# Optimization experiments

Hardware: AMD Instinct MI355X
Metric: run time of the kernel (lower is better)

## Reference

```python
import jax, jax.numpy as jnp
import numpy as np

EPS = 1e-7
K_IN, K_HID, K_OUT = 1.0, 1.1, 1.2
N_NODES, N_EDGES, IN_DIM, HID = 50000, 400000, 1024, 1024


def _expmap0(u, k):
    # u: tangent at origin with time component 0; u[:, 1:] are spatial coords
    sqrtK = jnp.sqrt(k)
    us = u[:, 1:]
    un = jnp.maximum(jnp.linalg.norm(us, axis=1, keepdims=True), EPS)
    t = un / sqrtK
    return jnp.concatenate([sqrtK * jnp.cosh(t), sqrtK * jnp.sinh(t) * us / un], axis=1)


def _logmap0(x, k):
    sqrtK = jnp.sqrt(k)
    x0, xs = x[:, 0:1], x[:, 1:]
    xn = jnp.maximum(jnp.linalg.norm(xs, axis=1, keepdims=True), EPS)
    theta = jnp.maximum(x0 / sqrtK, 1.0 + EPS)
    d = sqrtK * jnp.arccosh(theta)
    return jnp.concatenate([jnp.zeros_like(x0), d * xs / xn], axis=1)


def _proj(x, k):
    # re-fix the time component so <x,x>_L = -k
    xs = x[:, 1:]
    x0 = jnp.sqrt(k + jnp.sum(xs * xs, axis=1, keepdims=True))
    return jnp.concatenate([x0, xs], axis=1)


def _centroid(m, k):
    # Lorentzian centroid normalization: sqrt(k) * m / sqrt(|<m,m>_L|)
    l_inner = jnp.sum(m[:, 1:] ** 2, axis=1, keepdims=True) - m[:, 0:1] ** 2
    denom = jnp.sqrt(jnp.maximum(jnp.abs(l_inner), EPS))
    return jnp.sqrt(k) * m / denom


def _lgcn_conv(x, W, b, edge_src, edge_dst, edge_w, k_in, k_out):
    n = x.shape[0]
    # Lorentzian linear: logmap0 -> spatial matmul + bias -> expmap0
    u = _logmap0(x, k_in)[:, 1:]                      # [N, in_f]
    mx = u @ W.T + b                                  # [N, out_f-1]
    h = _expmap0(jnp.concatenate([jnp.zeros_like(mx[:, :1]), mx], axis=1), k_in)
    # sparse neighborhood aggregation + Lorentzian centroid
    msgs = edge_w[:, None] * h[edge_src]              # [E, out_f]
    m = jax.ops.segment_sum(msgs, edge_dst, num_segments=n)
    h = _centroid(m, k_in)
    # Lorentzian activation: relu in tangent space, re-exp on output manifold
    t = jax.nn.relu(_logmap0(h, k_in))                # time comp stays 0
    return _proj(_expmap0(t, k_out), k_out)


def setup_inputs() -> dict:
    key = jax.random.key(0)
    ks = jax.random.split(key, 8)
    x = jax.random.normal(ks[0], (N_NODES, IN_DIM), jnp.float32) * 0.01
    edge_src = jax.random.randint(ks[1], (N_EDGES,), 0, N_NODES, jnp.int32)
    edge_dst = jax.random.randint(ks[2], (N_EDGES,), 0, N_NODES, jnp.int32)
    edge_w = jax.random.uniform(ks[3], (N_EDGES,), jnp.float32)
    W1 = jax.random.normal(ks[4], (HID - 1, IN_DIM), jnp.float32) * 0.02
    b1 = jax.random.normal(ks[5], (HID - 1,), jnp.float32) * 0.01
    W2 = jax.random.normal(ks[6], (HID - 1, HID - 1), jnp.float32) * 0.02
    b2 = jax.random.normal(ks[7], (HID - 1,), jnp.float32) * 0.01
    return {"x": x, "edge_src": edge_src, "edge_dst": edge_dst, "edge_w": edge_w,
            "W1": W1, "b1": b1, "W2": W2, "b2": b2}


def reference(x, edge_src, edge_dst, edge_w, W1, b1, W2, b2):
    # encode(): prepend zero time coord, proj_tan0 (already 0), expmap0, proj
    x = jnp.concatenate([jnp.zeros_like(x[:, :1]), x], axis=1)  # [N, IN_DIM+1]
    xh = _proj(_expmap0(x, K_IN), K_IN)
    x1 = _lgcn_conv(xh, W1, b1, edge_src, edge_dst, edge_w, K_IN, K_HID)
    y = _lgcn_conv(x1, W2, b2, edge_src, edge_dst, edge_w, K_HID, K_OUT)
    return y
```

## Files before the change

kernel.cpp:

```cpp
#include <hip/hip_runtime.h>
#include <math.h>

#define EPSF 1e-7f
#define KPAD 1024
#define M_PAD 50176
#define NWG2 784

typedef __attribute__((ext_vector_type(8))) short bf16x8;
typedef __attribute__((ext_vector_type(4))) float f32x4;
typedef __attribute__((ext_vector_type(4))) unsigned short us4;
typedef __attribute__((ext_vector_type(8))) unsigned short us8;

__device__ inline unsigned short f2bf(float f) {
  unsigned u = __float_as_uint(f);
  return (unsigned short)((u + 0x7FFFu + ((u >> 16) & 1u)) >> 16);
}
__device__ inline float bf2f(unsigned short s) {
  return __uint_as_float(((unsigned)s) << 16);
}

__device__ inline void gload_lds16(const void* g, void* l) {
  __builtin_amdgcn_global_load_lds((const __attribute__((address_space(1))) void*)g,
                                   (__attribute__((address_space(3))) void*)l, 16, 0, 0);
}

__global__ __launch_bounds__(256) void cvt_rows_bf16(const float* __restrict__ x,
                                                     unsigned short* __restrict__ o) {
  int i = blockIdx.x, t = threadIdx.x;
  float4 v = *(const float4*)(x + (size_t)i * 1024 + 4 * t);
  us4 u = {f2bf(v.x), f2bf(v.y), f2bf(v.z), f2bf(v.w)};
  *(us4*)(o + (size_t)i * 1024 + 4 * t) = u;
}

__global__ __launch_bounds__(256) void cvt_w_bf16(const float* __restrict__ W,
                                                  unsigned short* __restrict__ o,
                                                  int rows, int cols) {
  int r = blockIdx.x, t = threadIdx.x;
  int c0 = 4 * t;
  us4 u;
#pragma unroll
  for (int j = 0; j < 4; ++j) {
    int c = c0 + j;
    float v = (r < rows && c < cols) ? W[(size_t)r * cols + c] : 0.0f;
    u[j] = f2bf(v);
  }
  *(us4*)(o + (size_t)r * 1024 + c0) = u;
}

__global__ __launch_bounds__(512, 2) void gemm_bt256(const unsigned short* __restrict__ A,
                                                     const unsigned short* __restrict__ B,
                                                     const float* __restrict__ bias,
                                                     unsigned short* __restrict__ C,
                                                     float* __restrict__ rowss) {
  __shared__ unsigned short lA[2 * 2 * 8192];
  __shared__ unsigned short lB[2 * 2 * 8192];
  const int wg = blockIdx.x;
  const int swz = (wg & 7) * 98 + (wg >> 3);
  const int bm = swz >> 2, bn = swz & 3;
  const int tid = threadIdx.x;
  const int wave = tid >> 6, lane = tid & 63;
  const int wr = wave >> 2, wc = wave & 3;
  const int fr = lane & 15, fg = lane >> 4;

  const unsigned short* Abase = A + (size_t)bm * 256 * KPAD;
  const unsigned short* Bbase = B + (size_t)bn * 256 * KPAD;

  const int aHalf = wr * 8192;
  const int bHalf = (wc >> 1) * 8192;
  const int lrB0 = (wc & 1) * 64;
  int ps[2];
#pragma unroll
  for (int s = 0; s < 2; ++s) ps[s] = (((s << 2) + fg) ^ (fr & 7)) << 3;

  const int sRow8 = lane >> 3;
  const int sDst = wave * 512 + lane * 8;
  const int sGran = ((lane & 7) ^ sRow8) << 3;

  f32x4 acc[8][4];
#pragma unroll
  for (int m = 0; m < 8; ++m)
#pragma unroll
    for (int n2 = 0; n2 < 4; ++n2) acc[m][n2] = (f32x4)0.0f;

  bf16x8 af[4][2], bf[4][2];

  auto STAGE_A = [&](int t, int h) {
    const int p = t & 1;
#pragma unroll
    for (int q = 0; q < 2; ++q) {
      int row = h * 128 + q * 64 + wave * 8 + sRow8;
      gload_lds16(Abase + (size_t)row * KPAD + t * 64 + sGran,
                  &lA[p * 16384 + h * 8192 + q * 4096 + sDst]);
    }
  };
  auto STAGE_B = [&](int t, int h) {
    const int p = t & 1;
#pragma unroll
    for (int q = 0; q < 2; ++q) {
      int row = h * 128 + q * 64 + wave * 8 + sRow8;
      gload_lds16(Bbase + (size_t)row * KPAD + t * 64 + sGran,
                  &lB[p * 16384 + h * 8192 + q * 4096 + sDst]);
    }
  };
  auto LDA4 = [&](int p, int mg) {
#pragma unroll
    for (int mi = 0; mi < 4; ++mi) {
      int ro = p * 16384 + aHalf + ((mg * 4 + mi) * 16 + fr) * 64;
#pragma unroll
      for (int s = 0; s < 2; ++s) af[mi][s] = *(const bf16x8*)&lA[ro + ps[s]];
    }
  };
  auto LDB2 = [&](int p, int ng) {
#pragma unroll
    for (int ni = 0; ni < 2; ++ni) {
      int ro = p * 16384 + bHalf + (lrB0 + (ng * 2 + ni) * 16 + fr) * 64;
#pragma unroll
      for (int s = 0; s < 2; ++s) bf[ng * 2 + ni][s] = *(const bf16x8*)&lB[ro + ps[s]];
    }
  };
  auto MM = [&](int mq, int nq) {
    __builtin_amdgcn_s_setprio(1);
#pragma unroll
    for (int mi = 0; mi < 4; ++mi)
#pragma unroll
      for (int ni = 0; ni < 2; ++ni)
#pragma unroll
        for (int s = 0; s < 2; ++s)
          acc[mq * 4 + mi][nq * 2 + ni] = __builtin_amdgcn_mfma_f32_16x16x32_bf16(
              af[mi][s], bf[nq * 2 + ni][s], acc[mq * 4 + mi][nq * 2 + ni], 0, 0, 0);
    __builtin_amdgcn_s_setprio(0);
  };
#define BAR() __builtin_amdgcn_s_barrier()

  STAGE_B(0, 0); STAGE_B(0, 1); STAGE_A(0, 0); STAGE_A(0, 1);
  STAGE_B(1, 0); STAGE_B(1, 1); STAGE_A(1, 0);
  asm volatile("s_waitcnt vmcnt(6)" ::: "memory");
  BAR();

#pragma unroll 1
  for (int it = 0; it < 7; ++it) {
    const int t0 = 2 * it, t1 = t0 + 1;
    LDA4(0, 0); LDB2(0, 0);
    STAGE_A(t1, 1);
    BAR(); MM(0, 0); BAR();
    LDB2(0, 1);
    BAR(); MM(0, 1); BAR();
    LDA4(0, 1);
    STAGE_B(t0 + 2, 0);
    BAR(); MM(1, 0); BAR();
    STAGE_B(t0 + 2, 1); STAGE_A(t0 + 2, 0);
    asm volatile("s_waitcnt vmcnt(6)" ::: "memory");
    BAR(); MM(1, 1); BAR();
    LDA4(1, 0); LDB2(1, 0);
    STAGE_A(t0 + 2, 1);
    BAR(); MM(0, 0); BAR();
    LDB2(1, 1);
    BAR(); MM(0, 1); BAR();
    LDA4(1, 1);
    STAGE_B(t1 + 2, 0);
    BAR(); MM(1, 0); BAR();
    STAGE_B(t1 + 2, 1); STAGE_A(t1 + 2, 0);
    asm volatile("s_waitcnt vmcnt(6)" ::: "memory");
    BAR(); MM(1, 1); BAR();
  }

  asm volatile("s_waitcnt vmcnt(0)" ::: "memory");
  BAR();
#pragma unroll
  for (int p = 0; p < 2; ++p) {
    LDA4(p, 0); LDB2(p, 0); MM(0, 0);
    LDB2(p, 1); MM(0, 1);
    LDA4(p, 1); MM(1, 0); MM(1, 1);
  }
#undef BAR

  const int crow0 = bm * 256 + wr * 128;
  const int ccol0 = bn * 256 + wc * 64;
  float rs[8][4];
#pragma unroll
  for (int m = 0; m < 8; ++m)
#pragma unroll
    for (int j = 0; j < 4; ++j) rs[m][j] = 0.0f;
#pragma unroll
  for (int m = 0; m < 8; ++m) {
#pragma unroll
    for (int n2 = 0; n2 < 4; ++n2) {
      int col = ccol0 + n2 * 16 + fr;
      float bv = (col < 1023) ? bias[col] : 0.0f;
      int row0 = crow0 + m * 16 + fg * 4;
      unsigned short* cp = C + (size_t)row0 * 1024 + col;
#pragma unroll
      for (int j = 0; j < 4; ++j) {
        float v = acc[m][n2][j] + bv;
        cp[(size_t)j * 1024] = f2bf(v);
        rs[m][j] += v * v;
      }
    }
  }
#pragma unroll
  for (int m = 0; m < 8; ++m)
#pragma unroll
    for (int j = 0; j < 4; ++j) {
      float v = rs[m][j];
      v += __shfl_xor(v, 1);
      v += __shfl_xor(v, 2);
      v += __shfl_xor(v, 4);
      v += __shfl_xor(v, 8);
      rs[m][j] = v;
    }
  __syncthreads();
  float* red = (float*)lA;
  if (fr == 0) {
#pragma unroll
    for (int m = 0; m < 8; ++m)
#pragma unroll
      for (int j = 0; j < 4; ++j)
        red[(wr * 128 + m * 16 + fg * 4 + j) * 4 + wc] = rs[m][j];
  }
  __syncthreads();
  if (tid < 256) {
    float s = red[tid * 4] + red[tid * 4 + 1] + red[tid * 4 + 2] + red[tid * 4 + 3];
    rowss[(size_t)(bm * 256 + tid) * 4 + bn] = s;
  }
}

__global__ __launch_bounds__(256) void row_finalize(const float* __restrict__ rowss,
                                                    unsigned short* __restrict__ raw,
                                                    float* __restrict__ sc_tab, float sqrtK,
                                                    int n) {
  int i = blockIdx.x * 256 + threadIdx.x;
  if (i >= n) return;
  float ss = rowss[4 * i] + rowss[4 * i + 1] + rowss[4 * i + 2] + rowss[4 * i + 3];
  float un = fmaxf(sqrtf(ss), EPSF);
  float tt = un / sqrtK;
  float e = expf(tt);
  float ch = 0.5f * (e + 1.0f / e), sh = 0.5f * (e - 1.0f / e);
  float h0 = sqrtK * ch, sc = sqrtK * sh / un;
  sc_tab[i] = sc;
  raw[(size_t)i * 1024 + 1023] = f2bf(h0 / sc);
}

__global__ __launch_bounds__(256) void deg_count(const int* __restrict__ ed, int* __restrict__ cnt,
                                                 int nE) {
  int i = blockIdx.x * 256 + threadIdx.x;
  if (i < nE) atomicAdd(&cnt[ed[i]], 1);
}

__global__ __launch_bounds__(256) void scan1(const int* __restrict__ cnt, int* __restrict__ excl,
                                             int* __restrict__ bsum, int n) {
  __shared__ int s[256];
  int t = threadIdx.x;
  int i = blockIdx.x * 256 + t;
  int v = (i < n) ? cnt[i] : 0;
  s[t] = v;
  __syncthreads();
#pragma unroll
  for (int o = 1; o < 256; o <<= 1) {
    int add = (t >= o) ? s[t - o] : 0;
    __syncthreads();
    s[t] += add;
    __syncthreads();
  }
  if (i < n) excl[i] = s[t] - v;
  if (t == 255) bsum[blockIdx.x] = s[t];
}

__global__ __launch_bounds__(256) void scan2(int* __restrict__ bsum, int* __restrict__ boff,
                                             int nb) {
  __shared__ int s[256];
  int t = threadIdx.x;
  int v = (t < nb) ? bsum[t] : 0;
  s[t] = v;
  __syncthreads();
#pragma unroll
  for (int o = 1; o < 256; o <<= 1) {
    int add = (t >= o) ? s[t - o] : 0;
    __syncthreads();
    s[t] += add;
    __syncthreads();
  }
  if (t < nb) boff[t] = s[t] - v;
}

__global__ __launch_bounds__(256) void scan3(int* __restrict__ excl, const int* __restrict__ boff,
                                             int* __restrict__ rowstart, int* __restrict__ fill,
                                             int n, int nE) {
  int i = blockIdx.x * 256 + threadIdx.x;
  if (i < n) {
    int v = excl[i] + boff[blockIdx.x];
    rowstart[i] = v;
    fill[i] = v;
  }
  if (i == 0) rowstart[n] = nE;
}

__global__ __launch_bounds__(256) void bucket_fill(const int* __restrict__ es,
                                                   const int* __restrict__ ed,
                                                   const float* __restrict__ ew,
                                                   int* __restrict__ fill,
                                                   int2* __restrict__ sedge, int nE) {
  int i = blockIdx.x * 256 + threadIdx.x;
  if (i < nE) {
    int d = ed[i];
    int pos = atomicAdd(&fill[d], 1);
    sedge[pos] = make_int2(es[i], __float_as_int(ew[i]));
  }
}

__device__ inline void gather_row_wave(const unsigned short* __restrict__ h,
                                       const float* __restrict__ sc,
                                       const int2* __restrict__ sedge, int j0, int j1,
                                       int lane, float* fa, float* fb) {
  const char* hb = (const char*)h;
  int j = j0;
  for (; j + 2 <= j1; j += 2) {
    int2 e0 = sedge[j], e1 = sedge[j + 1];
    float w0 = __int_as_float(e0.y) * sc[e0.x];
    float w1 = __int_as_float(e1.y) * sc[e1.x];
    const us8* p0 = (const us8*)(hb + (((unsigned)e0.x) << 11)) + lane;
    const us8* p1 = (const us8*)(hb + (((unsigned)e1.x) << 11)) + lane;
    us8 a0 = p0[0], b0 = p0[64];
    us8 a1 = p1[0], b1 = p1[64];
#pragma unroll
    for (int q = 0; q < 8; ++q) {
      fa[q] += w0 * bf2f(a0[q]) + w1 * bf2f(a1[q]);
      fb[q] += w0 * bf2f(b0[q]) + w1 * bf2f(b1[q]);
    }
  }
  if (j < j1) {
    int2 e = sedge[j];
    float w = __int_as_float(e.y) * sc[e.x];
    const us8* p = (const us8*)(hb + (((unsigned)e.x) << 11)) + lane;
    us8 a = p[0], b = p[64];
#pragma unroll
    for (int q = 0; q < 8; ++q) {
      fa[q] += w * bf2f(a[q]);
      fb[q] += w * bf2f(b[q]);
    }
  }
}

__device__ inline float wave_sum(float v) {
#pragma unroll
  for (int m = 1; m <= 32; m <<= 1) v += __shfl_xor(v, m);
  return v;
}

__global__ __launch_bounds__(256) void gather_centroid_tangent(
    const unsigned short* __restrict__ h, const float* __restrict__ sc,
    const int* __restrict__ rs, const int2* __restrict__ sedge,
    unsigned short* __restrict__ u16, float sqrtK, int n) {
  int wv = threadIdx.x >> 6, lane = threadIdx.x & 63;
  int i = blockIdx.x * 4 + wv;
  if (i >= n) return;
  int j0 = rs[i], j1 = rs[i + 1];
  float fa[8] = {0.f, 0.f, 0.f, 0.f, 0.f, 0.f, 0.f, 0.f};
  float fb[8] = {0.f, 0.f, 0.f, 0.f, 0.f, 0.f, 0.f, 0.f};
  gather_row_wave(h, sc, sedge, j0, j1, lane, fa, fb);
  float m0 = __shfl(fb[7], 63);
  if (lane == 63) fb[7] = 0.0f;
  float ssl = 0.f;
#pragma unroll
  for (int q = 0; q < 8; ++q) ssl += fa[q] * fa[q] + fb[q] * fb[q];
  float ss = wave_sum(ssl);

  float l = ss - m0 * m0;
  float denom = sqrtf(fmaxf(fabsf(l), EPSF));
  float c = sqrtK / denom;
  float xn = fmaxf(c * sqrtf(ss), EPSF);
  float theta = fmaxf(m0 / denom, 1.0f + EPSF);
  float d = sqrtK * acoshf(theta);
  float f = c * (d / xn);
  us8 ua, ub;
#pragma unroll
  for (int q = 0; q < 8; ++q) {
    ua[q] = f2bf(fmaxf(fa[q], 0.0f) * f);
    ub[q] = f2bf(fmaxf(fb[q], 0.0f) * f);
  }
  if (lane == 63) ub[7] = 0;
  unsigned short* o = u16 + (size_t)i * 1024 + lane * 8;
  *(us8*)o = ua;
  *(us8*)(o + 512) = ub;
}

__global__ __launch_bounds__(256) void gather_centroid_final(
    const unsigned short* __restrict__ h, const float* __restrict__ sc,
    const int* __restrict__ rs, const int2* __restrict__ sedge, float* __restrict__ y,
    float sqrtKin, float sqrtKout, int n) {
  int wv = threadIdx.x >> 6, lane = threadIdx.x & 63;
  int i = blockIdx.x * 4 + wv;
  if (i >= n) return;
  int j0 = rs[i], j1 = rs[i + 1];
  float fa[8] = {0.f, 0.f, 0.f, 0.f, 0.f, 0.f, 0.f, 0.f};
  float fb[8] = {0.f, 0.f, 0.f, 0.f, 0.f, 0.f, 0.f, 0.f};
  gather_row_wave(h, sc, sedge, j0, j1, lane, fa, fb);
  float m0 = __shfl(fb[7], 63);
  if (lane == 63) fb[7] = 0.0f;
  float ssl = 0.f;
#pragma unroll
  for (int q = 0; q < 8; ++q) ssl += fa[q] * fa[q] + fb[q] * fb[q];
  float ss = wave_sum(ssl);

  float l = ss - m0 * m0;
  float denom = sqrtf(fmaxf(fabsf(l), EPSF));
  float c = sqrtKin / denom;
  float xn = fmaxf(c * sqrtf(ss), EPSF);
  float theta = fmaxf(m0 / denom, 1.0f + EPSF);
  float d = sqrtKin * acoshf(theta);
  float f = c * (d / xn);
  float oa[8], ob[8];
  float ss2l = 0.f;
#pragma unroll
  for (int q = 0; q < 8; ++q) {
    oa[q] = fmaxf(fa[q], 0.0f) * f;
    ob[q] = fmaxf(fb[q], 0.0f) * f;
  }
  if (lane == 63) ob[7] = 0.0f;
#pragma unroll
  for (int q = 0; q < 8; ++q) ss2l += oa[q] * oa[q] + ob[q] * ob[q];
  float ss2 = wave_sum(ss2l);

  float un = fmaxf(sqrtf(ss2), EPSF);
  float tt = un / sqrtKout;
  float e = expf(tt);
  float ch = 0.5f * (e + 1.0f / e), sh = 0.5f * (e - 1.0f / e);
  float y0 = sqrtKout * ch, scale = sqrtKout * sh / un;
  float* yr = y + (size_t)i * 1024;
  int c0 = lane * 8;
#pragma unroll
  for (int q = 0; q < 8; ++q) {
    yr[1 + c0 + q] = scale * oa[q];
    int colb = 512 + c0 + q;
    if (colb < 1023) yr[1 + colb] = scale * ob[q];
  }
  if (lane == 0) yr[0] = y0;
}

extern "C" void kernel_launch(void* const* d_in, const int* in_sizes, int n_in,
                              void* d_out, int out_size, void* d_ws, size_t ws_size,
                              hipStream_t stream) {
  const float* x = (const float*)d_in[0];
  const int* es = (const int*)d_in[1];
  const int* ed = (const int*)d_in[2];
  const float* ew = (const float*)d_in[3];
  const float* W1 = (const float*)d_in[4];
  const float* b1 = (const float*)d_in[5];
  const float* W2 = (const float*)d_in[6];
  const float* b2 = (const float*)d_in[7];
  float* y = (float*)d_out;

  const int n = in_sizes[0] / 1024;
  const int nE = in_sizes[1];
  const int NB = (n + 255) / 256;
  const int EB = (nE + 255) / 256;

  char* ws = (char*)d_ws;
  size_t off = 0;
  auto alloc = [&](size_t bytes) {
    void* p = ws + off;
    off += (bytes + 255) & ~(size_t)255;
    return p;
  };
  unsigned short* u16 = (unsigned short*)alloc((size_t)M_PAD * 1024 * 2);
  unsigned short* w16 = (unsigned short*)alloc((size_t)1024 * 1024 * 2);
  unsigned short* raw16 = (unsigned short*)alloc((size_t)M_PAD * 1024 * 2);
  float* sc_tab = (float*)alloc((size_t)M_PAD * 4);
  float* rowss = (float*)alloc((size_t)M_PAD * 4 * 4);
  int* cnt = (int*)alloc((size_t)(n + 1) * 4);
  int* excl = (int*)alloc((size_t)n * 4);
  int* rowstart = (int*)alloc((size_t)(n + 1) * 4);
  int* fill = (int*)alloc((size_t)n * 4);
  int* bsum = (int*)alloc(256 * 4);
  int* boff = (int*)alloc(256 * 4);
  int2* sedge = (int2*)alloc((size_t)nE * 8);

  const float sK1 = 1.0f;
  const float sK2 = 1.0488088481701516f;
  const float sK3 = 1.0954451150103321f;

  const int GB = (n + 3) / 4;

  hipMemsetAsync(cnt, 0, (size_t)(n + 1) * 4, stream);
  deg_count<<<EB, 256, 0, stream>>>(ed, cnt, nE);
  scan1<<<NB, 256, 0, stream>>>(cnt, excl, bsum, n);
  scan2<<<1, 256, 0, stream>>>(bsum, boff, NB);
  scan3<<<NB, 256, 0, stream>>>(excl, boff, rowstart, fill, n, nE);
  bucket_fill<<<EB, 256, 0, stream>>>(es, ed, ew, fill, sedge, nE);

  cvt_rows_bf16<<<n, 256, 0, stream>>>(x, u16);
  cvt_w_bf16<<<1024, 256, 0, stream>>>(W1, w16, 1023, 1024);
  gemm_bt256<<<NWG2, 512, 0, stream>>>(u16, w16, b1, raw16, rowss);
  row_finalize<<<NB, 256, 0, stream>>>(rowss, raw16, sc_tab, sK1, n);
  gather_centroid_tangent<<<GB, 256, 0, stream>>>(raw16, sc_tab, rowstart, sedge, u16, sK1, n);

  cvt_w_bf16<<<1024, 256, 0, stream>>>(W2, w16, 1023, 1023);
  gemm_bt256<<<NWG2, 512, 0, stream>>>(u16, w16, b2, raw16, rowss);
  row_finalize<<<NB, 256, 0, stream>>>(rowss, raw16, sc_tab, sK2, n);
  gather_centroid_final<<<GB, 256, 0, stream>>>(raw16, sc_tab, rowstart, sedge, y, sK2, sK3, n);
}
```

Measured before the change: 686.2 us.

## Reschedule GEMM main loop to overlap LDS fragment reads with MFMA phases

Restructures the double-buffered bf16 GEMM main loop so LDS fragment reads for the next MFMA quadrant are issued right after the current MFMA block, inside the same barrier window. Global-to-LDS staging of the second B half is deferred and the vmcnt waits drop from 6 to 4. The prologue and epilogue are rewritten to match. The aim is to hide LDS read latency behind matrix-core work, at the cost of a more fragile ordering where buffer hazards between staged tiles and in-flight reads could appear.

```diff
diff --git a/kernel.cpp b/kernel.cpp
--- a/kernel.cpp
+++ b/kernel.cpp
@@ -102,7 +102,7 @@
                   &lB[p * 16384 + h * 8192 + q * 4096 + sDst]);
     }
   };
-  auto LDA4 = [&](int p, int mg) {
+  auto RD_A = [&](int p, int mg) {
 #pragma unroll
     for (int mi = 0; mi < 4; ++mi) {
       int ro = p * 16384 + aHalf + ((mg * 4 + mi) * 16 + fr) * 64;
@@ -110,7 +110,7 @@
       for (int s = 0; s < 2; ++s) af[mi][s] = *(const bf16x8*)&lA[ro + ps[s]];
     }
   };
-  auto LDB2 = [&](int p, int ng) {
+  auto RD_B = [&](int p, int ng) {
 #pragma unroll
     for (int ni = 0; ni < 2; ++ni) {
       int ro = p * 16384 + bHalf + (lrB0 + (ng * 2 + ni) * 16 + fr) * 64;
@@ -131,48 +131,47 @@
     __builtin_amdgcn_s_setprio(0);
   };
 #define BAR() __builtin_amdgcn_s_barrier()
+#define VMC(n) asm volatile("s_waitcnt vmcnt(" #n ")" ::: "memory")
 
   STAGE_B(0, 0); STAGE_B(0, 1); STAGE_A(0, 0); STAGE_A(0, 1);
-  STAGE_B(1, 0); STAGE_B(1, 1); STAGE_A(1, 0);
-  asm volatile("s_waitcnt vmcnt(6)" ::: "memory");
+  STAGE_B(1, 0); STAGE_A(1, 0);
+  VMC(4);
   BAR();
+  RD_A(0, 0); RD_B(0, 0);
 
 #pragma unroll 1
   for (int it = 0; it < 7; ++it) {
     const int t0 = 2 * it, t1 = t0 + 1;
-    LDA4(0, 0); LDB2(0, 0);
-    STAGE_A(t1, 1);
+    RD_B(0, 1); STAGE_A(t1, 1);
     BAR(); MM(0, 0); BAR();
-    LDB2(0, 1);
-    BAR(); MM(0, 1); BAR();
-    LDA4(0, 1);
+    STAGE_B(t1, 1);
+    BAR(); MM(0, 1); RD_A(0, 1); BAR();
     STAGE_B(t0 + 2, 0);
     BAR(); MM(1, 0); BAR();
-    STAGE_B(t0 + 2, 1); STAGE_A(t0 + 2, 0);
-    asm volatile("s_waitcnt vmcnt(6)" ::: "memory");
-    BAR(); MM(1, 1); BAR();
-    LDA4(1, 0); LDB2(1, 0);
-    STAGE_A(t0 + 2, 1);
+    STAGE_A(t0 + 2, 0); VMC(4);
+    BAR(); MM(1, 1); RD_A(1, 0); RD_B(1, 0); BAR();
+    RD_B(1, 1); STAGE_A(t0 + 2, 1);
     BAR(); MM(0, 0); BAR();
-    LDB2(1, 1);
-    BAR(); MM(0, 1); BAR();
-    LDA4(1, 1);
+    STAGE_B(t0 + 2, 1);
+    BAR(); MM(0, 1); RD_A(1, 1); BAR();
     STAGE_B(t1 + 2, 0);
     BAR(); MM(1, 0); BAR();
-    STAGE_B(t1 + 2, 1); STAGE_A(t1 + 2, 0);
-    asm volatile("s_waitcnt vmcnt(6)" ::: "memory");
-    BAR(); MM(1, 1); BAR();
-  }
-
-  asm volatile("s_waitcnt vmcnt(0)" ::: "memory");
-  BAR();
-#pragma unroll
-  for (int p = 0; p < 2; ++p) {
-    LDA4(p, 0); LDB2(p, 0); MM(0, 0);
-    LDB2(p, 1); MM(0, 1);
-    LDA4(p, 1); MM(1, 0); MM(1, 1);
-  }
+    STAGE_A(t1 + 2, 0); VMC(4);
+    BAR(); MM(1, 1); RD_A(0, 0); RD_B(0, 0); BAR();
+  }
+
+  RD_B(0, 1); STAGE_A(15, 1);
+  BAR(); MM(0, 0); BAR();
+  STAGE_B(15, 1);
+  BAR(); MM(0, 1); RD_A(0, 1); BAR();
+  BAR(); MM(1, 0); BAR();
+  VMC(0);
+  BAR(); MM(1, 1); RD_A(1, 0); RD_B(1, 0); BAR();
+  RD_B(1, 1); MM(0, 0);
+  MM(0, 1); RD_A(1, 1);
+  MM(1, 0); MM(1, 1);
 #undef BAR
+#undef VMC
 
   const int crow0 = bm * 256 + wr * 128;
   const int ccol0 = bn * 256 + wc * 64;
```

Measured after the change: 701.8 us. 1.02x slower.
